# Kernel optimization log

Hardware: AMD Instinct MI355X
Metric: run time of the kernel (lower is better)

Reference implementation:

```python
import jax, jax.numpy as jnp
import numpy as np

B, S, HID, H, D = 4, 1024, 2048, 16, 128
ROT = D // 2  # GLM 2D rotary: rotary dim is half the head dim (64)


def _rope_tables(seq_len, dim, base=10000.0):
    # dim = ROT; inv_freq over dim//2 frequencies, emb = cat(freqs, freqs)
    inv_freq = 1.0 / (base ** (jnp.arange(0, dim, 2, dtype=jnp.float32) / dim))
    t = jnp.arange(seq_len, dtype=jnp.float32)
    freqs = jnp.einsum('s,f->sf', t, inv_freq)          # [S, dim//2]
    emb = jnp.concatenate([freqs, freqs], axis=-1)       # [S, dim]
    return jnp.cos(emb), jnp.sin(emb)


def _rotate_half(x):
    x1, x2 = jnp.split(x, 2, axis=-1)
    return jnp.concatenate([-x2, x1], axis=-1)


def _apply_rope(x, cos, sin, pos_id):
    # x: [B,H,S,ROT]; pos_id: [B,S]; tables: [S,ROT]
    c = cos[pos_id][:, None, :, :]  # [B,1,S,ROT]
    s = sin[pos_id][:, None, :, :]
    return x * c + _rotate_half(x) * s


def setup_inputs() -> dict:
    key = jax.random.key(0)
    ks = jax.random.split(key, 12)
    w = 0.02
    inp = {
        'query': jax.random.normal(ks[0], (B, S, HID), jnp.float32),
        'key': jax.random.normal(ks[1], (B, S, HID), jnp.float32),
        'value': jax.random.normal(ks[2], (B, S, HID), jnp.float32),
        'mask': jnp.zeros((B, 1, S, S), jnp.float32),
        'position_bias': jax.random.normal(ks[3], (1, H, S, S), jnp.float32) * 0.1,
        'prev_attn': jax.random.normal(ks[4], (B, H, S, S), jnp.float32) * 0.1,
        'position_ids': jax.random.randint(ks[5], (B, 2, S), 0, S, jnp.int32),
        'Wq': jax.random.normal(ks[6], (HID, HID), jnp.float32) * w,
        'bq': jnp.zeros((HID,), jnp.float32),
        'Wk': jax.random.normal(ks[7], (HID, HID), jnp.float32) * w,
        'bk': jnp.zeros((HID,), jnp.float32),
        'Wv': jax.random.normal(ks[8], (HID, HID), jnp.float32) * w,
        'bv': jnp.zeros((HID,), jnp.float32),
        'Wo': jax.random.normal(ks[9], (HID, HID), jnp.float32) * w,
        'bo': jnp.zeros((HID,), jnp.float32),
    }
    return inp


def reference(query, key, value, mask, position_bias, prev_attn,
              Wq, bq, Wk, bk, Wv, bv, Wo, bo, position_ids):
    # QKV projections -> [B,H,S,D]
    def proj(x, W, b):
        return (x @ W.T + b).reshape(B, S, H, D).transpose(0, 2, 1, 3)
    q = proj(query, Wq, bq)
    k = proj(key, Wk, bk)
    v = proj(value, Wv, bv)

    # GLM 2D rotary: split head dim in halves, rope each with its own ids
    q1, q2 = jnp.split(q, 2, axis=-1)
    k1, k2 = jnp.split(k, 2, axis=-1)
    cos, sin = _rope_tables(S, ROT)
    pid = position_ids[:, 0, :]        # [B,S]
    bid = position_ids[:, 1, :]        # [B,S]
    q1 = _apply_rope(q1, cos, sin, pid)
    k1 = _apply_rope(k1, cos, sin, pid)
    q2 = _apply_rope(q2, cos, sin, bid)
    k2 = _apply_rope(k2, cos, sin, bid)
    q = jnp.concatenate([q1, q2], axis=-1)
    k = jnp.concatenate([k1, k2], axis=-1)

    scores = jnp.einsum('bhsd,bhtd->bhst', q, k)
    scores = scores + position_bias
    scores = scores / jnp.sqrt(jnp.float32(D))
    scores = scores + mask
    scores = scores + prev_attn          # residual attention accumulation
    prev_attn_out = scores
    probs = jax.nn.softmax(scores, axis=-1)
    ctx = jnp.einsum('bhst,bhtd->bhsd', probs, v)
    ctx = ctx.transpose(0, 2, 1, 3).reshape(B, S, HID)
    out = ctx @ Wo.T + bo
    return out, prev_attn_out
```

## Files before the change

### kernel.cpp

```cpp
#include <hip/hip_runtime.h>


#define B_  4
#define S_  1024
#define HID_ 2048
#define H_  16
#define D_  128
#define RSQRT_D 0.08838834764831845f

typedef _Float16 f16x8 __attribute__((ext_vector_type(8)));
typedef _Float16 f16x4 __attribute__((ext_vector_type(4)));
typedef float f32x4 __attribute__((ext_vector_type(4)));

#define MFMA16(a, b, c) __builtin_amdgcn_mfma_f32_16x16x32_f16(a, b, c, 0, 0, 0)

__device__ __forceinline__ void gll16(const void* g, void* l) {
  __builtin_amdgcn_global_load_lds(
      (const __attribute__((address_space(1))) void*)g,
      (__attribute__((address_space(3))) void*)l, 16, 0, 0);
}

__global__ void rope_table_kernel(float* __restrict__ tcos, float* __restrict__ tsin) {
  int i = blockIdx.x * blockDim.x + threadIdx.x;
  int pos = i >> 5, j = i & 31;
  float inv = expf(-(float)j * (9.210340371976184f / 32.0f));
  float ang = (float)pos * inv;
  tcos[i] = cosf(ang);
  tsin[i] = sinf(ang);
}

__global__ void cvt_kernel(const float* __restrict__ in, _Float16* __restrict__ out, int n8) {
  int i = blockIdx.x * blockDim.x + threadIdx.x;
  if (i >= n8) return;
  const f32x4* in4 = (const f32x4*)in;
  f32x4 a = in4[i * 2], b = in4[i * 2 + 1];
  f16x8 v;
  v[0] = (_Float16)a[0]; v[1] = (_Float16)a[1]; v[2] = (_Float16)a[2]; v[3] = (_Float16)a[3];
  v[4] = (_Float16)b[0]; v[5] = (_Float16)b[1]; v[6] = (_Float16)b[2]; v[7] = (_Float16)b[3];
  *(f16x8*)(out + (size_t)i * 8) = v;
}

template <int MODE>
__global__ __launch_bounds__(256) void proj_kernel(
    const _Float16* __restrict__ A, const _Float16* __restrict__ Bw,
    const float* __restrict__ bias, void* __restrict__ outp,
    const int* __restrict__ pids, const float* __restrict__ tcos,
    const float* __restrict__ tsin) {
  constexpr int N = HID_, K = HID_;
  constexpr int BK = 64;
  __shared__ _Float16 As[128 * BK];
  __shared__ _Float16 Bs[128 * BK];

  const int tid = threadIdx.x;
  const int bid = (blockIdx.x & 7) * 64 + (blockIdx.x >> 3);
  const int tm = bid >> 4, tn = bid & 15;
  const int m0 = tm * 128, n0 = tn * 128;
  const int w = tid >> 6, l = tid & 63;
  const int mw = (w >> 1) * 64, nw = (w & 1) * 64;
  const int lr = l & 15, lh = l >> 4;

  f32x4 acc[4][4] = {};

  for (int kt = 0; kt < K / BK; ++kt) {
    const int k0 = kt * BK;
    __syncthreads();
#pragma unroll
    for (int i = 0; i < 4; ++i) {
      const int e = i * 2048 + tid * 8;
      gll16(A + (size_t)(m0 + (e >> 6)) * K + k0 + (e & 63), As + e);
      gll16(Bw + (size_t)(n0 + (e >> 6)) * K + k0 + (e & 63), Bs + e);
    }
    asm volatile("s_waitcnt vmcnt(0)" ::: "memory");
    __syncthreads();
#pragma unroll
    for (int kk = 0; kk < 2; ++kk) {
      f16x8 af[4], bf[4];
#pragma unroll
      for (int mi = 0; mi < 4; ++mi)
        af[mi] = *(const f16x8*)(As + (mw + mi * 16 + lr) * BK + kk * 32 + lh * 8);
#pragma unroll
      for (int ni = 0; ni < 4; ++ni)
        bf[ni] = *(const f16x8*)(Bs + (nw + ni * 16 + lr) * BK + kk * 32 + lh * 8);
#pragma unroll
      for (int mi = 0; mi < 4; ++mi)
#pragma unroll
        for (int ni = 0; ni < 4; ++ni)
          acc[mi][ni] = MFMA16(af[mi], bf[ni], acc[mi][ni]);
    }
  }

  if constexpr (MODE == 2) {
    float* out = (float*)outp;
#pragma unroll
    for (int mi = 0; mi < 4; ++mi)
#pragma unroll
      for (int ni = 0; ni < 4; ++ni) {
        const int col = n0 + nw + ni * 16 + lr;
        const float bb = bias[col];
#pragma unroll
        for (int r = 0; r < 4; ++r) {
          const int row = m0 + mw + mi * 16 + lh * 4 + r;
          out[(size_t)row * N + col] = acc[mi][ni][r] + bb;
        }
      }
  } else if constexpr (MODE == 1) {
    _Float16* out = (_Float16*)outp;
#pragma unroll
    for (int mi = 0; mi < 4; ++mi)
#pragma unroll
      for (int ni = 0; ni < 4; ++ni) {
        const int col = n0 + nw + ni * 16 + lr;
        const float bb = bias[col];
        const int h = col >> 7, hd = col & 127;
#pragma unroll
        for (int r = 0; r < 4; ++r) {
          const int row = m0 + mw + mi * 16 + lh * 4 + r;
          const int b = row >> 10, s = row & 1023;
          out[(((size_t)(b * H_ + h)) * D_ + hd) * S_ + s] = (_Float16)(acc[mi][ni][r] + bb);
        }
      }
  } else {
    _Float16* out = (_Float16*)outp;
    const int sel = (nw >> 6) & 1;
#pragma unroll
    for (int mi = 0; mi < 4; ++mi) {
#pragma unroll
      for (int r = 0; r < 4; ++r) {
        const int row = m0 + mw + mi * 16 + lh * 4 + r;
        const int b = row >> 10, s = row & 1023;
        const int pos = pids[b * 2 * S_ + sel * S_ + s];
#pragma unroll
        for (int ni = 0; ni < 2; ++ni) {
          const int col = n0 + nw + ni * 16 + lr;
          const int j = ni * 16 + lr;
          const float c = tcos[pos * 32 + j];
          const float sn = tsin[pos * 32 + j];
          const float x1 = acc[mi][ni][r] + bias[col];
          const float x2 = acc[mi][ni + 2][r] + bias[col + 32];
          const int h = col >> 7, hd = col & 127;
          const size_t base = (((size_t)(b * H_ + h)) * S_ + s) * D_;
          out[base + hd] = (_Float16)(x1 * c - x2 * sn);
          out[base + hd + 32] = (_Float16)(x2 * c + x1 * sn);
        }
      }
    }
  }
}

__global__ __launch_bounds__(256) void flash_kernel(
    const _Float16* __restrict__ q, const _Float16* __restrict__ k,
    const _Float16* __restrict__ vt, const float* __restrict__ pbias,
    const float* __restrict__ maskp, const float* __restrict__ prev,
    float* __restrict__ scores, _Float16* __restrict__ ctx) {
  constexpr int BT = 64;
  __shared__ _Float16 Ks[BT * D_];
  __shared__ _Float16 VTs[D_ * BT];
  __shared__ _Float16 Ps[4][16 * BT];

  const int tid = threadIdx.x, w = tid >> 6, l = tid & 63;
  const int lr = l & 15, lh = l >> 4;
  const int sid = (blockIdx.x & 7) * 128 + (blockIdx.x >> 3);
  const int qt = sid & 15, byh = sid >> 4;
  const int b = byh >> 4, h = byh & 15;
  const size_t plane = (size_t)byh;
  const int q0 = qt * 64 + w * 16;
  const int qrow = q0 + lr;
  const int swz = (lr & 7) << 3;

  const float* prow  = prev  + (plane * S_ + qrow) * S_;
  const float* pbrow = pbias + ((size_t)h * S_ + qrow) * S_;
  const float* mrow  = maskp + ((size_t)b * S_ + qrow) * S_;
  float*       srow  = scores + (plane * S_ + qrow) * S_;

  f16x8 qa[4];
#pragma unroll
  for (int kk = 0; kk < 4; ++kk)
    qa[kk] = *(const f16x8*)(q + (plane * S_ + qrow) * D_ + kk * 32 + lh * 8);

  f32x4 o[8] = {};
  float m_r = -1e30f, l_r = 0.0f;

  for (int tt = 0; tt < S_ / BT; ++tt) {
    const int t0 = tt * BT;
    __syncthreads();
#pragma unroll
    for (int i = 0; i < 4; ++i) {
      const int e = i * 2048 + tid * 8;
      const int krow = e >> 7;
      gll16(k + (plane * S_ + t0 + krow) * D_ + ((e & 127) ^ ((krow & 7) << 3)), Ks + e);
      const int vrow = e >> 6;
      gll16(vt + (plane * D_ + vrow) * S_ + t0 + ((e & 63) ^ ((vrow & 7) << 3)), VTs + e);
    }
    f32x4 pv4[4], pb4[4], mk4[4];
#pragma unroll
    for (int nt = 0; nt < 4; ++nt) {
      const int toff = t0 + nt * 16 + lh * 4;
      pv4[nt] = __builtin_nontemporal_load((const f32x4*)(prow + toff));
      pb4[nt] = *(const f32x4*)(pbrow + toff);
      mk4[nt] = *(const f32x4*)(mrow + toff);
    }
    asm volatile("s_waitcnt vmcnt(0)" ::: "memory");
    __syncthreads();

    f32x4 sa[4] = {};
    __builtin_amdgcn_s_setprio(1);
#pragma unroll
    for (int nt = 0; nt < 4; ++nt)
#pragma unroll
      for (int kk = 0; kk < 4; ++kk) {
        const int row = nt * 16 + lr;
        f16x8 kb = *(const f16x8*)(Ks + row * D_ + ((kk * 32 + lh * 8) ^ swz));
        sa[nt] = MFMA16(kb, qa[kk], sa[nt]);
      }
    __builtin_amdgcn_s_setprio(0);

#pragma unroll
    for (int nt = 0; nt < 4; ++nt) {
      const int toff = t0 + nt * 16 + lh * 4;
      f32x4 sc4 = (sa[nt] + pb4[nt]) * RSQRT_D + mk4[nt] + pv4[nt];
      __builtin_nontemporal_store(sc4, (f32x4*)(srow + toff));
      sa[nt] = sc4;
    }

    float tmx = -1e30f;
#pragma unroll
    for (int nt = 0; nt < 4; ++nt)
#pragma unroll
      for (int r = 0; r < 4; ++r) tmx = fmaxf(tmx, sa[nt][r]);
    tmx = fmaxf(tmx, __shfl_xor(tmx, 16));
    tmx = fmaxf(tmx, __shfl_xor(tmx, 32));
    if (!__all(tmx <= m_r + 8.0f)) {
      const float newm = fmaxf(m_r, tmx);
      const float al = __expf(m_r - newm);
      m_r = newm;
      l_r *= al;
#pragma unroll
      for (int nd = 0; nd < 8; ++nd) o[nd] *= al;
    }
    float ts = 0.0f;
#pragma unroll
    for (int nt = 0; nt < 4; ++nt)
#pragma unroll
      for (int r = 0; r < 4; ++r) {
        const float pe = __expf(sa[nt][r] - m_r);
        sa[nt][r] = pe;
        ts += pe;
      }
    ts += __shfl_xor(ts, 16);
    ts += __shfl_xor(ts, 32);
    l_r += ts;

    _Float16* pw = &Ps[w][0];
#pragma unroll
    for (int nt = 0; nt < 4; ++nt) {
      f16x4 pk;
      pk[0] = (_Float16)sa[nt][0]; pk[1] = (_Float16)sa[nt][1];
      pk[2] = (_Float16)sa[nt][2]; pk[3] = (_Float16)sa[nt][3];
      *(f16x4*)(pw + lr * BT + ((nt * 16 + lh * 4) ^ swz)) = pk;
    }

    __builtin_amdgcn_s_setprio(1);
#pragma unroll
    for (int kk = 0; kk < 2; ++kk) {
      const f16x8 pa = *(const f16x8*)(pw + lr * BT + ((kk * 32 + lh * 8) ^ swz));
#pragma unroll
      for (int nd = 0; nd < 8; ++nd) {
        const int vr = nd * 16 + lr;
        const f16x8 vb = *(const f16x8*)(VTs + vr * BT + ((kk * 32 + lh * 8) ^ swz));
        o[nd] = MFMA16(vb, pa, o[nd]);
      }
    }
    __builtin_amdgcn_s_setprio(0);
  }

  const float inv_l = 1.0f / l_r;
  _Float16* crow = ctx + ((size_t)(b * S_) + qrow) * HID_ + h * D_;
#pragma unroll
  for (int nd = 0; nd < 8; ++nd) {
    f16x4 cv;
#pragma unroll
    for (int r = 0; r < 4; ++r) cv[r] = (_Float16)(o[nd][r] * inv_l);
    *(f16x4*)(crow + nd * 16 + lh * 4) = cv;
  }
}

extern "C" void kernel_launch(void* const* d_in, const int* in_sizes, int n_in,
                              void* d_out, int out_size, void* d_ws, size_t ws_size,
                              hipStream_t stream) {
  const float* query = (const float*)d_in[0];
  const float* key_i = (const float*)d_in[1];
  const float* value = (const float*)d_in[2];
  const float* maskp = (const float*)d_in[3];
  const float* pbias = (const float*)d_in[4];
  const float* prev  = (const float*)d_in[5];
  const int*   pids  = (const int*)d_in[6];
  const float* Wq = (const float*)d_in[7];
  const float* bq = (const float*)d_in[8];
  const float* Wk = (const float*)d_in[9];
  const float* bk = (const float*)d_in[10];
  const float* Wv = (const float*)d_in[11];
  const float* bv = (const float*)d_in[12];
  const float* Wo = (const float*)d_in[13];
  const float* bo = (const float*)d_in[14];

  char* ws = (char*)d_ws;
  const size_t OFF_TCOS = 0;
  const size_t OFF_TSIN = 131072;
  const size_t OFF_W    = 262144;
  const size_t OFF_X    = OFF_W + 4ull * 8388608;
  const size_t OFF_Q    = OFF_X + 3ull * 16777216;
  const size_t OFF_K    = OFF_Q + 16777216;
  const size_t OFF_VT   = OFF_K + 16777216;
  const size_t OFF_CTX  = OFF_X + 16777216;

  float* tcos = (float*)(ws + OFF_TCOS);
  float* tsin = (float*)(ws + OFF_TSIN);
  _Float16* Wq16 = (_Float16*)(ws + OFF_W);
  _Float16* Wk16 = (_Float16*)(ws + OFF_W + 8388608);
  _Float16* Wv16 = (_Float16*)(ws + OFF_W + 2ull * 8388608);
  _Float16* Wo16 = (_Float16*)(ws + OFF_W + 3ull * 8388608);
  _Float16* Xq16 = (_Float16*)(ws + OFF_X);
  _Float16* Xk16 = (_Float16*)(ws + OFF_X + 16777216);
  _Float16* Xv16 = (_Float16*)(ws + OFF_X + 2ull * 16777216);
  _Float16* q16  = (_Float16*)(ws + OFF_Q);
  _Float16* k16  = (_Float16*)(ws + OFF_K);
  _Float16* vt16 = (_Float16*)(ws + OFF_VT);
  _Float16* ctx16 = (_Float16*)(ws + OFF_CTX);

  float* out_f32 = (float*)d_out;
  float* scores  = (float*)d_out + 8388608;

  rope_table_kernel<<<128, 256, 0, stream>>>(tcos, tsin);

  cvt_kernel<<<2048, 256, 0, stream>>>(Wq, Wq16, 524288);
  cvt_kernel<<<2048, 256, 0, stream>>>(Wk, Wk16, 524288);
  cvt_kernel<<<2048, 256, 0, stream>>>(Wv, Wv16, 524288);
  cvt_kernel<<<2048, 256, 0, stream>>>(Wo, Wo16, 524288);
  cvt_kernel<<<4096, 256, 0, stream>>>(query, Xq16, 1048576);
  cvt_kernel<<<4096, 256, 0, stream>>>(key_i, Xk16, 1048576);
  cvt_kernel<<<4096, 256, 0, stream>>>(value, Xv16, 1048576);

  proj_kernel<0><<<512, 256, 0, stream>>>(Xq16, Wq16, bq, (void*)q16, pids, tcos, tsin);
  proj_kernel<0><<<512, 256, 0, stream>>>(Xk16, Wk16, bk, (void*)k16, pids, tcos, tsin);
  proj_kernel<1><<<512, 256, 0, stream>>>(Xv16, Wv16, bv, (void*)vt16, nullptr, nullptr, nullptr);

  flash_kernel<<<1024, 256, 0, stream>>>(q16, k16, vt16, pbias, maskp, prev,
                                         scores, ctx16);

  proj_kernel<2><<<512, 256, 0, stream>>>(ctx16, Wo16, bo, (void*)out_f32,
                                          nullptr, nullptr, nullptr);
}
```

Before: 480.4 us.

## Prefetch next K/V tile and prev_attn into registers during compute

Replaces the per-iteration direct global-to-LDS loads with a register-staged software pipeline. The first K/V tile and prev_attn slice are loaded before the loop, and each iteration issues global loads for the next tile into registers. Those registers are written into LDS after the PV MFMAs, between two barriers. This is meant to hide global load latency behind the QK and PV compute, at the cost of extra VGPRs (kreg/vreg/pvB), which may reduce occupancy, plus an extra barrier and LDS write pass per tile.

```diff
diff --git a/kernel.cpp b/kernel.cpp
--- a/kernel.cpp
+++ b/kernel.cpp
@@ -180,27 +180,47 @@
   f32x4 o[8] = {};
   float m_r = -1e30f, l_r = 0.0f;
 
+#pragma unroll
+  for (int i = 0; i < 4; ++i) {
+    const int e = i * 2048 + tid * 8;
+    const int krow = e >> 7;
+    gll16(k + (plane * S_ + krow) * D_ + ((e & 127) ^ ((krow & 7) << 3)), Ks + e);
+    const int vrow = e >> 6;
+    gll16(vt + (plane * D_ + vrow) * S_ + ((e & 63) ^ ((vrow & 7) << 3)), VTs + e);
+  }
+  f32x4 pvA[4];
+#pragma unroll
+  for (int nt = 0; nt < 4; ++nt)
+    pvA[nt] = __builtin_nontemporal_load((const f32x4*)(prow + nt * 16 + lh * 4));
+  asm volatile("s_waitcnt vmcnt(0)" ::: "memory");
+  __syncthreads();
+
   for (int tt = 0; tt < S_ / BT; ++tt) {
     const int t0 = tt * BT;
-    __syncthreads();
+    const int t1 = (tt < 15) ? t0 + BT : 0;
+
+    f32x4 pb4[4], mk4[4];
+#pragma unroll
+    for (int nt = 0; nt < 4; ++nt) {
+      const int toff = t0 + nt * 16 + lh * 4;
+      pb4[nt] = *(const f32x4*)(pbrow + toff);
+      mk4[nt] = *(const f32x4*)(mrow + toff);
+    }
+    f32x4 pvB[4];
+#pragma unroll
+    for (int nt = 0; nt < 4; ++nt)
+      pvB[nt] = __builtin_nontemporal_load((const f32x4*)(prow + t1 + nt * 16 + lh * 4));
+    f16x8 kreg[4], vreg[4];
 #pragma unroll
     for (int i = 0; i < 4; ++i) {
       const int e = i * 2048 + tid * 8;
       const int krow = e >> 7;
-      gll16(k + (plane * S_ + t0 + krow) * D_ + ((e & 127) ^ ((krow & 7) << 3)), Ks + e);
+      kreg[i] = *(const f16x8*)(k + (plane * S_ + t1 + krow) * D_ +
+                                ((e & 127) ^ ((krow & 7) << 3)));
       const int vrow = e >> 6;
-      gll16(vt + (plane * D_ + vrow) * S_ + t0 + ((e & 63) ^ ((vrow & 7) << 3)), VTs + e);
-    }
-    f32x4 pv4[4], pb4[4], mk4[4];
-#pragma unroll
-    for (int nt = 0; nt < 4; ++nt) {
-      const int toff = t0 + nt * 16 + lh * 4;
-      pv4[nt] = __builtin_nontemporal_load((const f32x4*)(prow + toff));
-      pb4[nt] = *(const f32x4*)(pbrow + toff);
-      mk4[nt] = *(const f32x4*)(mrow + toff);
-    }
-    asm volatile("s_waitcnt vmcnt(0)" ::: "memory");
-    __syncthreads();
+      vreg[i] = *(const f16x8*)(vt + (plane * D_ + vrow) * S_ + t1 +
+                                ((e & 63) ^ ((vrow & 7) << 3)));
+    }
 
     f32x4 sa[4] = {};
     __builtin_amdgcn_s_setprio(1);
@@ -217,7 +237,7 @@
 #pragma unroll
     for (int nt = 0; nt < 4; ++nt) {
       const int toff = t0 + nt * 16 + lh * 4;
-      f32x4 sc4 = (sa[nt] + pb4[nt]) * RSQRT_D + mk4[nt] + pv4[nt];
+      f32x4 sc4 = (sa[nt] + pb4[nt]) * RSQRT_D + mk4[nt] + pvA[nt];
       __builtin_nontemporal_store(sc4, (f32x4*)(srow + toff));
       sa[nt] = sc4;
     }
@@ -271,6 +291,17 @@
       }
     }
     __builtin_amdgcn_s_setprio(0);
+
+    __syncthreads();
+#pragma unroll
+    for (int i = 0; i < 4; ++i) {
+      const int e = i * 2048 + tid * 8;
+      *(f16x8*)(Ks + e) = kreg[i];
+      *(f16x8*)(VTs + e) = vreg[i];
+    }
+    __syncthreads();
+#pragma unroll
+    for (int nt = 0; nt < 4; ++nt) pvA[nt] = pvB[nt];
   }
 
   const float inv_l = 1.0f / l_r;
```

Result: slower. 521.8 us (+8.6%).
